# Kernel optimization log

Hardware: AMD Instinct MI355X
Metric: run time of the kernel (lower is better)

Reference implementation:

```python
import jax, jax.numpy as jnp
import numpy as np

LN_EPS = 1e-5

def _layernorm(x, g, b):
    mu = jnp.mean(x, axis=-1, keepdims=True)
    var = jnp.var(x, axis=-1, keepdims=True)
    return (x - mu) / jnp.sqrt(var + LN_EPS) * g + b

def setup_inputs() -> dict:
    key = jax.random.key(0)
    ks = jax.random.split(key, 12)
    N, D_WSI, D_OMIC, D, DH = 50000, 1024, 1577, 256, 128
    def rn(k, shape, s=0.02):
        return jax.random.normal(k, shape, jnp.float32) * s
    return {
        'wsi': jax.random.normal(ks[0], (N, D_WSI), jnp.float32),
        'x_omic': jax.random.normal(ks[1], (D_OMIC,), jnp.float32),
        # SNNOmics: Linear(1577,256)+ELU, Linear(256,256)+ELU (AlphaDropout=eval identity)
        'W1': rn(ks[2], (D_OMIC, 256)), 'b1': jnp.zeros((256,), jnp.float32),
        'W2': rn(ks[3], (256, 256)), 'b2': jnp.zeros((256,), jnp.float32),
        # wsi projection Linear(1024,256)
        'Wp': rn(ks[4], (D_WSI, D)), 'bp': jnp.zeros((D,), jnp.float32),
        # MMAttentionLayer pre-norm (dim=256)
        'ln1_g': jnp.ones((D,), jnp.float32), 'ln1_b': jnp.zeros((D,), jnp.float32),
        # to_qkv: Linear(256, 3*heads*dim_head) = Linear(256, 384), no bias (heads=1, dim_head=128)
        'Wqkv': rn(ks[5], (D, 3 * DH)),
        # FeedForward(dim=128, mult=1): LN + Linear(128,128)+GELU+Linear(128,128) (no residual)
        'ln2_g': jnp.ones((DH,), jnp.float32), 'ln2_b': jnp.zeros((DH,), jnp.float32),
        'Wf1': rn(ks[6], (DH, DH)), 'bf1': jnp.zeros((DH,), jnp.float32),
        'Wf2': rn(ks[7], (DH, DH)), 'bf2': jnp.zeros((DH,), jnp.float32),
        # final LayerNorm(128)
        'ln3_g': jnp.ones((DH,), jnp.float32), 'ln3_b': jnp.zeros((DH,), jnp.float32),
        # to_logits: Linear(256,64)+ReLU+Linear(64,4)
        'Wl1': rn(ks[8], (2 * DH, 64)), 'bl1': jnp.zeros((64,), jnp.float32),
        'Wl2': rn(ks[9], (64, 4)), 'bl2': jnp.zeros((4,), jnp.float32),
    }

def reference(wsi, x_omic, W1, b1, W2, b2, Wp, bp, ln1_g, ln1_b, Wqkv,
              ln2_g, ln2_b, Wf1, bf1, Wf2, bf2, ln3_g, ln3_b, Wl1, bl1, Wl2, bl2):
    M = 1            # num_pathways
    DH = 128         # dim_head (heads=1)
    scale = DH ** -0.5
    # SNN omics encoder -> one pathway token [1, 256]
    h = jax.nn.elu(x_omic @ W1 + b1)
    h = jax.nn.elu(h @ W2 + b2)
    h_omic = h[None, :]                              # [1, 256]
    # WSI projection -> histology tokens [N, 256]
    wsi_embed = wsi @ Wp + bp                        # [N, 256]
    tokens = jnp.concatenate([h_omic, wsi_embed], axis=0)   # [1+N, 256]
    # MMAttentionLayer: pre-norm then asymmetric pathway/histology attention
    xn = _layernorm(tokens, ln1_g, ln1_b)
    qkv = xn @ Wqkv                                  # [1+N, 384]
    q, k, v = jnp.split(qkv, 3, axis=-1)             # each [1+N, 128]
    q = q * scale
    q_p, q_h = q[:M], q[M:]                          # [1,128], [N,128]
    k_p, k_h = k[:M], k[M:]
    # cross attention: histology -> pathways (rows of length M=1)
    cross_attn_hist = q_h @ k_p.T                    # [N, 1]
    cross_attn_hist = jax.nn.softmax(cross_attn_hist, axis=-1)
    # pathway row attends to [pathways | histology]
    attn_p = q_p @ k_p.T                             # [1, 1]
    cross_attn_p = q_p @ k_h.T                       # [1, N]
    attn_ph = jax.nn.softmax(jnp.concatenate([attn_p, cross_attn_p], axis=-1), axis=-1)  # [1, 1+N]
    out_p = attn_ph @ v                              # [1, 128]
    out_h = cross_attn_hist @ v[:M]                  # [N, 128]
    out = jnp.concatenate([out_p, out_h], axis=0)    # [1+N, 128] (residual=False: no conv)
    # FeedForward (no residual add in original) + LayerNorm
    mm = _layernorm(out, ln2_g, ln2_b)
    mm = jax.nn.gelu(mm @ Wf1 + bf1, approximate=False) @ Wf2 + bf2
    mm = _layernorm(mm, ln3_g, ln3_b)                # [1+N, 128]
    paths_embed = jnp.mean(mm[:M], axis=0)           # [128]
    wsi_embed_post = jnp.mean(mm[M:], axis=0)        # [128]
    embedding = jnp.concatenate([paths_embed, wsi_embed_post])[None, :]  # [1, 256]
    logits = jax.nn.relu(embedding @ Wl1 + bl1) @ Wl2 + bl2              # [1, 4]
    prob = jax.nn.softmax(logits, axis=-1)
    return logits, prob
```

## Files before the change

kernel.cpp:

```cpp
#include <hip/hip_runtime.h>
#include <hip/hip_bf16.h>
#include <math.h>

#define LN_EPS 1e-5f

typedef unsigned short ushortT;
typedef short bf16x8 __attribute__((ext_vector_type(8)));
typedef float f32x4 __attribute__((ext_vector_type(4)));

#define WS_QP   0
#define WS_V0   128
#define WS_S0   256
#define WS_H1P  512
#define WS_PART 4608
#define PART_STRIDE 132
#define PART_M 128
#define PART_L 129
#define WS_GP   109000
#define GP_STRIDE 132
#define NCOMB   32
#define WS_WPT  131072
#define WS_WKVT 262144

__device__ __forceinline__ float elu1(float x){ return x > 0.f ? x : expm1f(x); }
__device__ __forceinline__ unsigned pk2(float lo, float hi){
  union { __hip_bfloat162 h; unsigned u; } cv;
  cv.h = __float22bfloat162_rn(make_float2(lo, hi));
  return cv.u;
}
__device__ __forceinline__ void dma16(const void* g, void* l) {
  __builtin_amdgcn_global_load_lds(
      (const __attribute__((address_space(1))) unsigned int*)g,
      (__attribute__((address_space(3))) unsigned int*)l, 16, 0, 0);
}
template<int N> __device__ __forceinline__ void vwait() {
  asm volatile("s_waitcnt vmcnt(%0)" :: "i"(N) : "memory");
}
__device__ __forceinline__ void lwait0() {
  asm volatile("s_waitcnt lgkmcnt(0)" ::: "memory");
}
__device__ __forceinline__ void sbar()   { __builtin_amdgcn_s_barrier(); }
__device__ __forceinline__ void schedb() { __builtin_amdgcn_sched_barrier(0); }

__global__ __launch_bounds__(256) void k_setup(
    const float* __restrict__ Wp, const float* __restrict__ Wqkv,
    const float* __restrict__ x, const float* __restrict__ W1, int d_omic,
    ushortT* __restrict__ wpt, ushortT* __restrict__ wkvt, float* __restrict__ ws)
{
  int bb = blockIdx.x, t = threadIdx.x;
  if (bb < 32) {
    int kc = bb, m = t, sw = (m >> 1) & 3;
    #pragma unroll
    for (int c = 0; c < 4; ++c) {
      float v[8];
      #pragma unroll
      for (int e = 0; e < 8; ++e) v[e] = Wp[(size_t)(kc * 32 + c * 8 + e) * 256 + m];
      uint4 w = make_uint4(pk2(v[0], v[1]), pk2(v[2], v[3]), pk2(v[4], v[5]), pk2(v[6], v[7]));
      *(uint4*)&wpt[kc * 8192 + m * 32 + ((c ^ sw) * 8)] = w;
    }
  } else if (bb < 40) {
    int kk = bb - 32, m = t, sw = (m >> 1) & 3;
    #pragma unroll
    for (int c = 0; c < 4; ++c) {
      float v[8];
      #pragma unroll
      for (int e = 0; e < 8; ++e) v[e] = Wqkv[(size_t)(kk * 32 + c * 8 + e) * 384 + 128 + m];
      uint4 w = make_uint4(pk2(v[0], v[1]), pk2(v[2], v[3]), pk2(v[4], v[5]), pk2(v[6], v[7]));
      *(uint4*)&wkvt[kk * 8192 + m * 32 + ((c ^ sw) * 8)] = w;
    }
  } else {
    int g = bb - 40;
    int i0 = g * 99, i1 = min(i0 + 99, d_omic);
    __shared__ float xs[112];
    for (int i = i0 + t; i < i1; i += 256) xs[i - i0] = x[i];
    __syncthreads();
    float s = 0.f;
    for (int i = i0; i < i1; i++) s = fmaf(xs[i - i0], W1[(size_t)i * 256 + t], s);
    ws[WS_H1P + g * 256 + t] = s;
  }
}

__global__ __launch_bounds__(256) void k_omic(
    const float* __restrict__ b1,
    const float* __restrict__ W2, const float* __restrict__ b2,
    const float* __restrict__ Wqkv,
    const float* __restrict__ ln1_g, const float* __restrict__ ln1_b,
    float* __restrict__ ws)
{
  __shared__ float h1[256];
  __shared__ float xn0[256];
  __shared__ float qs[128], ks[128];
  __shared__ float red[8];
  int tid = threadIdx.x, lane = tid & 63, wave = tid >> 6;

  float s = b1[tid];
  for (int g = 0; g < 16; g++) s += ws[WS_H1P + g * 256 + tid];
  h1[tid] = elu1(s);
  __syncthreads();

  s = b2[tid];
  for (int i = 0; i < 256; i++) s = fmaf(h1[i], W2[i * 256 + tid], s);
  float t0 = elu1(s);

  float ps = t0, pq = t0 * t0;
  for (int m = 1; m < 64; m <<= 1) { ps += __shfl_xor(ps, m); pq += __shfl_xor(pq, m); }
  if (lane == 0) { red[wave] = ps; red[4 + wave] = pq; }
  __syncthreads();
  float mu = (red[0] + red[1] + red[2] + red[3]) * (1.f / 256.f);
  float var = (red[4] + red[5] + red[6] + red[7]) * (1.f / 256.f) - mu * mu;
  float xn = (t0 - mu) * rsqrtf(var + LN_EPS) * ln1_g[tid] + ln1_b[tid];
  xn0[tid] = xn;
  __syncthreads();

  float a = 0.f;
  for (int j = 0; j < 256; j++) a = fmaf(xn0[j], Wqkv[j * 384 + tid], a);
  if (tid < 128) { float q = a * 0.088388347648318447f; qs[tid] = q; ws[WS_QP + tid] = q; }
  else           { ks[tid - 128] = a; }
  if (tid < 128) {
    float av = 0.f;
    for (int j = 0; j < 256; j++) av = fmaf(xn0[j], Wqkv[j * 384 + 256 + tid], av);
    ws[WS_V0 + tid] = av;
  }
  __syncthreads();
  float p = (tid < 128) ? qs[tid] * ks[tid] : 0.f;
  for (int m = 1; m < 64; m <<= 1) p += __shfl_xor(p, m);
  if (lane == 0) red[wave] = p;
  __syncthreads();
  if (tid == 0) ws[WS_S0] = red[0] + red[1] + red[2] + red[3];
}

__global__ __launch_bounds__(512, 4) void k_main(
    const float* __restrict__ wsi, int N,
    const ushortT* __restrict__ wpt, const ushortT* __restrict__ wkvt,
    const float* __restrict__ bp,
    const float* __restrict__ ln1_g, const float* __restrict__ ln1_b,
    float* __restrict__ ws)
{
  __shared__ __align__(16) char U[81920];

  const int tid = threadIdx.x;
  const int lane = tid & 63, wv = tid >> 6;
  const int l15 = lane & 15, lh = lane >> 4;
  const int cg = wv & 3, rg = wv >> 2;
  const int b = blockIdx.x, r0 = b * 128;

  int wsiSrc[2];
  #pragma unroll
  for (int i = 0; i < 2; ++i) {
    int rowL = 16 * wv + 8 * i + (lane >> 3);
    int gr = r0 + rowL; gr = (gr < N) ? gr : (N - 1);
    wsiSrc[i] = gr * 1024 + (((lane & 7) ^ (lane >> 3)) << 2);
  }
  int wptSrc[2];
  #pragma unroll
  for (int j = 0; j < 2; ++j) wptSrc[j] = (32 * wv + 16 * j) * 32 + lane * 8;

  const unsigned afslot = (unsigned)((lh ^ ((l15 >> 1) & 3)) << 4);
  const unsigned bs0 = (unsigned)(((2 * lh)     ^ (l15 & 7)) << 4);
  const unsigned bs1 = (unsigned)(((2 * lh + 1) ^ (l15 & 7)) << 4);

  const f32x4 z4 = {0.f, 0.f, 0.f, 0.f};
  f32x4 acc[4][4];
  #pragma unroll
  for (int mt = 0; mt < 4; ++mt)
    #pragma unroll
    for (int nt = 0; nt < 4; ++nt) acc[mt][nt] = z4;

  auto stageWsi = [&](int kc, int slot) {
    char* ds = U + slot * 16384 + wv * 2048;
    #pragma unroll
    for (int i = 0; i < 2; ++i) dma16(wsi + wsiSrc[i] + kc * 32, ds + i * 1024);
  };
  auto stageWpt = [&](int kc, int slot) {
    char* dw = U + 49152 + slot * 16384 + wv * 2048;
    #pragma unroll
    for (int j = 0; j < 2; ++j) dma16(wpt + wptSrc[j] + kc * 8192, dw + j * 1024);
  };

  stageWsi(0, 0); stageWpt(0, 0);
  stageWsi(1, 1); stageWpt(1, 1);
  stageWsi(2, 2);
  for (int s = 0; s < 32; ++s) {
    if (s < 30) vwait<6>(); else if (s == 30) vwait<4>(); else vwait<0>();
    sbar(); schedb();
    {
      const char* Ws = U + (s % 3) * 16384;
      const char* Wf = U + 49152 + (s & 1) * 16384;
      bf16x8 af[4], bfr[4];
      #pragma unroll
      for (int mt = 0; mt < 4; ++mt)
        af[mt] = *(const bf16x8*)(Wf + (64 * cg + 16 * mt + l15) * 64 + afslot);
      #pragma unroll
      for (int nt = 0; nt < 4; ++nt) {
        const char* p = Ws + (64 * rg + 16 * nt + l15) * 128;
        uint4 ua = *(const uint4*)(p + bs0);
        uint4 ub = *(const uint4*)(p + bs1);
        union { unsigned u[4]; bf16x8 v; } cv;
        cv.u[0] = pk2(__uint_as_float(ua.x), __uint_as_float(ua.y));
        cv.u[1] = pk2(__uint_as_float(ua.z), __uint_as_float(ua.w));
        cv.u[2] = pk2(__uint_as_float(ub.x), __uint_as_float(ub.y));
        cv.u[3] = pk2(__uint_as_float(ub.z), __uint_as_float(ub.w));
        bfr[nt] = cv.v;
      }
      #pragma unroll
      for (int mt = 0; mt < 4; ++mt)
        #pragma unroll
        for (int nt = 0; nt < 4; ++nt)
          acc[mt][nt] = __builtin_amdgcn_mfma_f32_16x16x32_bf16(af[mt], bfr[nt], acc[mt][nt], 0, 0, 0);
    }
    sbar(); schedb();
    if (s < 30) stageWpt(s + 2, s & 1);
    if (s < 29) stageWsi(s + 3, s % 3);
  }

  float* red = (float*)(U + 65536);
  float4 bp4[4], g4[4], b4[4];
  #pragma unroll
  for (int mt = 0; mt < 4; ++mt) {
    int m0 = 64 * cg + 16 * mt + 4 * lh;
    bp4[mt] = *(const float4*)&bp[m0];
    g4[mt]  = *(const float4*)&ln1_g[m0];
    b4[mt]  = *(const float4*)&ln1_b[m0];
  }
  float ps[4], pq[4];
  #pragma unroll
  for (int nt = 0; nt < 4; ++nt) { ps[nt] = 0.f; pq[nt] = 0.f; }
  #pragma unroll
  for (int mt = 0; mt < 4; ++mt) {
    const float bb4[4] = {bp4[mt].x, bp4[mt].y, bp4[mt].z, bp4[mt].w};
    #pragma unroll
    for (int nt = 0; nt < 4; ++nt)
      #pragma unroll
      for (int r = 0; r < 4; ++r) {
        float v = acc[mt][nt][r] + bb4[r];
        acc[mt][nt][r] = v;
        ps[nt] += v; pq[nt] += v * v;
      }
  }
  #pragma unroll
  for (int nt = 0; nt < 4; ++nt) {
    ps[nt] += __shfl_xor(ps[nt], 16); pq[nt] += __shfl_xor(pq[nt], 16);
    ps[nt] += __shfl_xor(ps[nt], 32); pq[nt] += __shfl_xor(pq[nt], 32);
  }
  if (lh == 0) {
    #pragma unroll
    for (int nt = 0; nt < 4; ++nt) {
      int row = 64 * rg + 16 * nt + l15;
      *(float2*)&red[row * 8 + cg * 2] = make_float2(ps[nt], pq[nt]);
    }
  }
  lwait0(); sbar(); schedb();
  float mu[4], rstd[4];
  #pragma unroll
  for (int nt = 0; nt < 4; ++nt) {
    int row = 64 * rg + 16 * nt + l15;
    float s_ = 0.f, q_ = 0.f;
    #pragma unroll
    for (int c = 0; c < 4; ++c) { s_ += red[row * 8 + c * 2]; q_ += red[row * 8 + c * 2 + 1]; }
    float m_ = s_ * (1.f / 256.f);
    float v_ = q_ * (1.f / 256.f) - m_ * m_;
    mu[nt] = m_; rstd[nt] = rsqrtf(v_ + LN_EPS);
  }
  #pragma unroll
  for (int nt = 0; nt < 4; ++nt) {
    int row = 64 * rg + 16 * nt + l15;
    unsigned rswz = (unsigned)((row & 7) << 4);
    #pragma unroll
    for (int mt = 0; mt < 4; ++mt) {
      float x0 = (acc[mt][nt][0] - mu[nt]) * rstd[nt] * g4[mt].x + b4[mt].x;
      float x1 = (acc[mt][nt][1] - mu[nt]) * rstd[nt] * g4[mt].y + b4[mt].y;
      float x2 = (acc[mt][nt][2] - mu[nt]) * rstd[nt] * g4[mt].z + b4[mt].z;
      float x3 = (acc[mt][nt][3] - mu[nt]) * rstd[nt] * g4[mt].w + b4[mt].w;
      unsigned off = (unsigned)(row * 512 + (64 * cg + 16 * mt + 4 * lh) * 2) ^ rswz;
      *(uint2*)(U + off) = make_uint2(pk2(x0, x1), pk2(x2, x3));
    }
  }
  lwait0(); sbar(); schedb();

  f32x4 acc2[4][4];
  #pragma unroll
  for (int mt = 0; mt < 4; ++mt)
    #pragma unroll
    for (int nt = 0; nt < 4; ++nt) acc2[mt][nt] = z4;
  int kvBase[4];
  #pragma unroll
  for (int mt = 0; mt < 4; ++mt) {
    int m = 64 * cg + 16 * mt + l15;
    kvBase[mt] = m * 32 + ((lh ^ ((m >> 1) & 3)) << 3);
  }
  bf16x8 gA[4], gB[4];
  #pragma unroll
  for (int mt = 0; mt < 4; ++mt) gA[mt] = *(const bf16x8*)(wkvt + kvBase[mt]);
  #pragma unroll
  for (int kp = 0; kp < 4; ++kp) {
    const int kk0 = 2 * kp, kk1 = 2 * kp + 1;
    #pragma unroll
    for (int mt = 0; mt < 4; ++mt)
      gB[mt] = *(const bf16x8*)(wkvt + kvBase[mt] + kk1 * 8192);
    {
      bf16x8 bfr[4];
      #pragma unroll
      for (int nt = 0; nt < 4; ++nt) {
        int row = 64 * rg + 16 * nt + l15;
        unsigned off = (unsigned)(row * 512 + kk0 * 64 + lh * 16) ^ (unsigned)((row & 7) << 4);
        bfr[nt] = *(const bf16x8*)(U + off);
      }
      #pragma unroll
      for (int mt = 0; mt < 4; ++mt)
        #pragma unroll
        for (int nt = 0; nt < 4; ++nt)
          acc2[mt][nt] = __builtin_amdgcn_mfma_f32_16x16x32_bf16(gA[mt], bfr[nt], acc2[mt][nt], 0, 0, 0);
    }
    if (kp < 3) {
      #pragma unroll
      for (int mt = 0; mt < 4; ++mt)
        gA[mt] = *(const bf16x8*)(wkvt + kvBase[mt] + (kk0 + 2) * 8192);
    }
    {
      bf16x8 bfr[4];
      #pragma unroll
      for (int nt = 0; nt < 4; ++nt) {
        int row = 64 * rg + 16 * nt + l15;
        unsigned off = (unsigned)(row * 512 + kk1 * 64 + lh * 16) ^ (unsigned)((row & 7) << 4);
        bfr[nt] = *(const bf16x8*)(U + off);
      }
      #pragma unroll
      for (int mt = 0; mt < 4; ++mt)
        #pragma unroll
        for (int nt = 0; nt < 4; ++nt)
          acc2[mt][nt] = __builtin_amdgcn_mfma_f32_16x16x32_bf16(gB[mt], bfr[nt], acc2[mt][nt], 0, 0, 0);
    }
  }
  sbar(); schedb();

  float* sred = (float*)U;
  float* aux  = (float*)(U + 1024);
  float* wts  = (float*)(U + 1056);
  float* vred = (float*)(U + 1600);
  float* part = ws + WS_PART + (size_t)b * PART_STRIDE;

  if (cg < 2) {
    float4 qp4[4];
    #pragma unroll
    for (int mt = 0; mt < 4; ++mt)
      qp4[mt] = *(const float4*)&ws[WS_QP + 64 * cg + 16 * mt + 4 * lh];
    float sp[4];
    #pragma unroll
    for (int nt = 0; nt < 4; ++nt) {
      float s_ = 0.f;
      #pragma unroll
      for (int mt = 0; mt < 4; ++mt) {
        s_ = fmaf(qp4[mt].x, acc2[mt][nt][0], s_);
        s_ = fmaf(qp4[mt].y, acc2[mt][nt][1], s_);
        s_ = fmaf(qp4[mt].z, acc2[mt][nt][2], s_);
        s_ = fmaf(qp4[mt].w, acc2[mt][nt][3], s_);
      }
      sp[nt] = s_;
    }
    #pragma unroll
    for (int nt = 0; nt < 4; ++nt) {
      sp[nt] += __shfl_xor(sp[nt], 16);
      sp[nt] += __shfl_xor(sp[nt], 32);
    }
    if (lh == 0) {
      #pragma unroll
      for (int nt = 0; nt < 4; ++nt) sred[cg * 128 + 64 * rg + 16 * nt + l15] = sp[nt];
    }
  }
  lwait0(); sbar(); schedb();

  float sv = -INFINITY, ev = 0.f;
  if (tid < 128) {
    sv = sred[tid] + sred[128 + tid];
    if (r0 + tid >= N) sv = -INFINITY;
  }
  float mb = sv;
  #pragma unroll
  for (int m = 1; m < 64; m <<= 1) mb = fmaxf(mb, __shfl_xor(mb, m));
  if (tid < 128 && lane == 0) aux[tid >> 6] = mb;
  lwait0(); sbar(); schedb();
  float M2 = fmaxf(aux[0], aux[1]);
  if (tid < 128) { ev = (r0 + tid < N) ? expf(sv - M2) : 0.f; wts[tid] = ev; }
  float lsum = ev;
  #pragma unroll
  for (int m = 1; m < 64; m <<= 1) lsum += __shfl_xor(lsum, m);
  if (tid < 128 && lane == 0) aux[2 + (tid >> 6)] = lsum;
  lwait0(); sbar(); schedb();
  if (tid == 0) { part[PART_M] = M2; part[PART_L] = aux[2] + aux[3]; }

  if (cg >= 2) {
    float wr[4];
    #pragma unroll
    for (int nt = 0; nt < 4; ++nt) wr[nt] = wts[64 * rg + 16 * nt + l15];
    #pragma unroll
    for (int mt = 0; mt < 4; ++mt) {
      float vs0 = 0.f, vs1 = 0.f, vs2 = 0.f, vs3 = 0.f;
      #pragma unroll
      for (int nt = 0; nt < 4; ++nt) {
        vs0 = fmaf(wr[nt], acc2[mt][nt][0], vs0);
        vs1 = fmaf(wr[nt], acc2[mt][nt][1], vs1);
        vs2 = fmaf(wr[nt], acc2[mt][nt][2], vs2);
        vs3 = fmaf(wr[nt], acc2[mt][nt][3], vs3);
      }
      #pragma unroll
      for (int m = 1; m < 16; m <<= 1) {
        vs0 += __shfl_xor(vs0, m); vs1 += __shfl_xor(vs1, m);
        vs2 += __shfl_xor(vs2, m); vs3 += __shfl_xor(vs3, m);
      }
      if (l15 == 0)
        *(float4*)&vred[128 * rg + 64 * (cg - 2) + 16 * mt + 4 * lh] =
            make_float4(vs0, vs1, vs2, vs3);
    }
  }
  lwait0(); sbar(); schedb();
  if (tid < 128) part[tid] = vred[tid] + vred[128 + tid];
}

__global__ __launch_bounds__(128) void k_fin1(float* __restrict__ ws, int NB, int chunk)
{
  int g = blockIdx.x, col = threadIdx.x;
  int c0 = g * chunk, c1 = min(c0 + chunk, NB);
  const float* part = ws + WS_PART;
  float mg = -INFINITY;
  for (int bb = c0; bb < c1; ++bb)
    mg = fmaxf(mg, part[(size_t)bb * PART_STRIDE + PART_M]);
  float a = 0.f, lg = 0.f;
  for (int bb = c0; bb < c1; ++bb) {
    float w = expf(part[(size_t)bb * PART_STRIDE + PART_M] - mg);
    a  = fmaf(part[(size_t)bb * PART_STRIDE + col], w, a);
    lg = fmaf(part[(size_t)bb * PART_STRIDE + PART_L], w, lg);
  }
  ws[WS_GP + g * GP_STRIDE + col] = a;
  if (col == 0) {
    ws[WS_GP + g * GP_STRIDE + 128] = mg;
    ws[WS_GP + g * GP_STRIDE + 129] = lg;
  }
}

__global__ __launch_bounds__(256) void k_final(
    const float* __restrict__ ws,
    const float* __restrict__ Wf1, const float* __restrict__ bf1,
    const float* __restrict__ Wf2, const float* __restrict__ bf2,
    const float* __restrict__ ln2_g, const float* __restrict__ ln2_b,
    const float* __restrict__ ln3_g, const float* __restrict__ ln3_b,
    const float* __restrict__ Wl1, const float* __restrict__ bl1,
    const float* __restrict__ Wl2, const float* __restrict__ bl2,
    float* __restrict__ out)
{
  __shared__ float rowb[2][128];
  __shared__ float mmb[2][128];
  __shared__ float red[8];
  __shared__ float emb[256];
  __shared__ float abuf[64];
  __shared__ float lbuf[4];
  __shared__ float wg[NCOMB];
  __shared__ float MLs[2];
  int tid = threadIdx.x, lane = tid & 63, wave = tid >> 6;
  float s0 = ws[WS_S0];

  if (tid == 0) {
    float M = s0;
    for (int g = 0; g < NCOMB; ++g) M = fmaxf(M, ws[WS_GP + g * GP_STRIDE + 128]);
    float L = expf(s0 - M);
    for (int g = 0; g < NCOMB; ++g)
      L = fmaf(ws[WS_GP + g * GP_STRIDE + 129], expf(ws[WS_GP + g * GP_STRIDE + 128] - M), L);
    MLs[0] = M; MLs[1] = L;
  }
  __syncthreads();
  float M = MLs[0], L = MLs[1];
  if (tid < NCOMB) wg[tid] = expf(ws[WS_GP + tid * GP_STRIDE + 128] - M);
  __syncthreads();

  if (tid < 128) {
    float v0 = ws[WS_V0 + tid];
    float a = v0 * expf(s0 - M);
    #pragma unroll
    for (int g = 0; g < NCOMB; ++g) a = fmaf(ws[WS_GP + g * GP_STRIDE + tid], wg[g], a);
    rowb[0][tid] = a / L;
    rowb[1][tid] = v0;
  }
  __syncthreads();

  int row = tid >> 7, k = tid & 127;
  float x = rowb[row][k];
  float ps = x, pq = x * x;
  for (int m = 1; m < 64; m <<= 1) { ps += __shfl_xor(ps, m); pq += __shfl_xor(pq, m); }
  __syncthreads();
  if (lane == 0) { red[wave] = ps; red[4 + wave] = pq; }
  __syncthreads();
  {
    float sum = red[row * 2] + red[row * 2 + 1];
    float sq  = red[4 + row * 2] + red[4 + row * 2 + 1];
    float mu = sum * (1.f / 128.f);
    float var = sq * (1.f / 128.f) - mu * mu;
    x = (x - mu) * rsqrtf(var + LN_EPS) * ln2_g[k] + ln2_b[k];
  }
  mmb[row][k] = x;
  __syncthreads();
  float t1 = bf1[k];
  for (int j = 0; j < 128; j++) t1 = fmaf(mmb[row][j], Wf1[j * 128 + k], t1);
  float gg = t1 * 0.5f * (1.f + erff(t1 * 0.70710678118654752f));
  __syncthreads();
  rowb[row][k] = gg;
  __syncthreads();
  float t2 = bf2[k];
  for (int j = 0; j < 128; j++) t2 = fmaf(rowb[row][j], Wf2[j * 128 + k], t2);
  ps = t2; pq = t2 * t2;
  for (int m = 1; m < 64; m <<= 1) { ps += __shfl_xor(ps, m); pq += __shfl_xor(pq, m); }
  __syncthreads();
  if (lane == 0) { red[wave] = ps; red[4 + wave] = pq; }
  __syncthreads();
  {
    float sum = red[row * 2] + red[row * 2 + 1];
    float sq  = red[4 + row * 2] + red[4 + row * 2 + 1];
    float mu = sum * (1.f / 128.f);
    float var = sq * (1.f / 128.f) - mu * mu;
    t2 = (t2 - mu) * rsqrtf(var + LN_EPS) * ln3_g[k] + ln3_b[k];
  }
  emb[row * 128 + k] = t2;
  __syncthreads();
  if (tid < 64) {
    float a = bl1[tid];
    for (int j = 0; j < 256; j++) a = fmaf(emb[j], Wl1[j * 64 + tid], a);
    abuf[tid] = fmaxf(a, 0.f);
  }
  __syncthreads();
  if (tid < 4) {
    float lg = bl2[tid];
    for (int j = 0; j < 64; j++) lg = fmaf(abuf[j], Wl2[j * 4 + tid], lg);
    lbuf[tid] = lg;
  }
  __syncthreads();
  if (tid < 4) {
    float m4 = fmaxf(fmaxf(lbuf[0], lbuf[1]), fmaxf(lbuf[2], lbuf[3]));
    float e0 = expf(lbuf[0] - m4), e1 = expf(lbuf[1] - m4);
    float e2 = expf(lbuf[2] - m4), e3 = expf(lbuf[3] - m4);
    float ssum = e0 + e1 + e2 + e3;
    out[tid] = lbuf[tid];
    out[4 + tid] = expf(lbuf[tid] - m4) / ssum;
  }
}

extern "C" void kernel_launch(void* const* d_in, const int* in_sizes, int n_in,
                              void* d_out, int out_size, void* d_ws, size_t ws_size,
                              hipStream_t stream) {
  const float* wsi    = (const float*)d_in[0];
  const float* x_omic = (const float*)d_in[1];
  const float* W1     = (const float*)d_in[2];
  const float* b1     = (const float*)d_in[3];
  const float* W2     = (const float*)d_in[4];
  const float* b2     = (const float*)d_in[5];
  const float* Wp     = (const float*)d_in[6];
  const float* bp     = (const float*)d_in[7];
  const float* ln1_g  = (const float*)d_in[8];
  const float* ln1_b  = (const float*)d_in[9];
  const float* Wqkv   = (const float*)d_in[10];
  const float* ln2_g  = (const float*)d_in[11];
  const float* ln2_b  = (const float*)d_in[12];
  const float* Wf1    = (const float*)d_in[13];
  const float* bf1    = (const float*)d_in[14];
  const float* Wf2    = (const float*)d_in[15];
  const float* bf2    = (const float*)d_in[16];
  const float* ln3_g  = (const float*)d_in[17];
  const float* ln3_b  = (const float*)d_in[18];
  const float* Wl1    = (const float*)d_in[19];
  const float* bl1    = (const float*)d_in[20];
  const float* Wl2    = (const float*)d_in[21];
  const float* bl2    = (const float*)d_in[22];
  float* ws   = (float*)d_ws;
  float* outp = (float*)d_out;
  ushortT* wpt  = (ushortT*)(ws + WS_WPT);
  ushortT* wkvt = (ushortT*)(ws + WS_WKVT);

  int N = in_sizes[0] / 1024;
  int d_omic = in_sizes[1];
  int NB = (N + 127) / 128;
  int chunk = (NB + NCOMB - 1) / NCOMB;

  k_setup<<<56, 256, 0, stream>>>(Wp, Wqkv, x_omic, W1, d_omic, wpt, wkvt, ws);
  k_omic<<<1, 256, 0, stream>>>(b1, W2, b2, Wqkv, ln1_g, ln1_b, ws);
  k_main<<<NB, 512, 0, stream>>>(wsi, N, wpt, wkvt, bp, ln1_g, ln1_b, ws);
  k_fin1<<<NCOMB, 128, 0, stream>>>(ws, NB, chunk);
  k_final<<<1, 256, 0, stream>>>(ws, Wf1, bf1, Wf2, bf2, ln2_g, ln2_b,
                                 ln3_g, ln3_b, Wl1, bl1, Wl2, bl2, outp);
}
```

Baseline: 135.9 us.

## Fold K/V projections algebraically, removing per-row second GEMM in main kernel

Computes z = Wk·q once in the omic kernel, so attention scores become dot products of the normalized 256-d rows with z. The per-block weighted sum is accumulated over the 256-d normalized rows instead of projected V, and the V projection is applied only once to the combined softmax-weighted vector in the final kernel. This removes the second per-row MFMA GEMM, the bf16 staging of normalized rows to LDS and the Wkv transpose setup. In exchange, partial buffers double in width (256 instead of 128), and scores now use fp32 normalized rows rather than bf16 products, which changes rounding slightly.

Result: slower. 141.7 us (+4.2%).

```diff
diff --git a/kernel.cpp b/kernel.cpp
--- a/kernel.cpp
+++ b/kernel.cpp
@@ -13,14 +13,14 @@
 #define WS_S0   256
 #define WS_H1P  512
 #define WS_PART 4608
-#define PART_STRIDE 132
-#define PART_M 128
-#define PART_L 129
+#define PART_STRIDE 260
+#define PART_M 256
+#define PART_L 257
+#define WS_Z    107000
 #define WS_GP   109000
-#define GP_STRIDE 132
+#define GP_STRIDE 260
 #define NCOMB   32
 #define WS_WPT  131072
-#define WS_WKVT 262144
 
 __device__ __forceinline__ float elu1(float x){ return x > 0.f ? x : expm1f(x); }
 __device__ __forceinline__ unsigned pk2(float lo, float hi){
@@ -43,9 +43,9 @@
 __device__ __forceinline__ void schedb() { __builtin_amdgcn_sched_barrier(0); }
 
 __global__ __launch_bounds__(256) void k_setup(
-    const float* __restrict__ Wp, const float* __restrict__ Wqkv,
+    const float* __restrict__ Wp,
     const float* __restrict__ x, const float* __restrict__ W1, int d_omic,
-    ushortT* __restrict__ wpt, ushortT* __restrict__ wkvt, float* __restrict__ ws)
+    ushortT* __restrict__ wpt, float* __restrict__ ws)
 {
   int bb = blockIdx.x, t = threadIdx.x;
   if (bb < 32) {
@@ -58,18 +58,8 @@
       uint4 w = make_uint4(pk2(v[0], v[1]), pk2(v[2], v[3]), pk2(v[4], v[5]), pk2(v[6], v[7]));
       *(uint4*)&wpt[kc * 8192 + m * 32 + ((c ^ sw) * 8)] = w;
     }
-  } else if (bb < 40) {
-    int kk = bb - 32, m = t, sw = (m >> 1) & 3;
-    #pragma unroll
-    for (int c = 0; c < 4; ++c) {
-      float v[8];
-      #pragma unroll
-      for (int e = 0; e < 8; ++e) v[e] = Wqkv[(size_t)(kk * 32 + c * 8 + e) * 384 + 128 + m];
-      uint4 w = make_uint4(pk2(v[0], v[1]), pk2(v[2], v[3]), pk2(v[4], v[5]), pk2(v[6], v[7]));
-      *(uint4*)&wkvt[kk * 8192 + m * 32 + ((c ^ sw) * 8)] = w;
-    }
   } else {
-    int g = bb - 40;
+    int g = bb - 32;
     int i0 = g * 99, i1 = min(i0 + 99, d_omic);
     __shared__ float xs[112];
     for (int i = i0 + t; i < i1; i += 256) xs[i - i0] = x[i];
@@ -127,11 +117,23 @@
   if (lane == 0) red[wave] = p;
   __syncthreads();
   if (tid == 0) ws[WS_S0] = red[0] + red[1] + red[2] + red[3];
+
+  float zv = 0.f;
+  #pragma unroll 4
+  for (int d = 0; d < 128; d += 4) {
+    float4 q4 = *(const float4*)&qs[d];
+    const float* wr_ = &Wqkv[tid * 384 + 128 + d];
+    zv = fmaf(q4.x, wr_[0], zv);
+    zv = fmaf(q4.y, wr_[1], zv);
+    zv = fmaf(q4.z, wr_[2], zv);
+    zv = fmaf(q4.w, wr_[3], zv);
+  }
+  ws[WS_Z + tid] = zv;
 }
 
 __global__ __launch_bounds__(512, 4) void k_main(
     const float* __restrict__ wsi, int N,
-    const ushortT* __restrict__ wpt, const ushortT* __restrict__ wkvt,
+    const ushortT* __restrict__ wpt,
     const float* __restrict__ bp,
     const float* __restrict__ ln1_g, const float* __restrict__ ln1_b,
     float* __restrict__ ws)
@@ -159,12 +161,12 @@
   const unsigned bs0 = (unsigned)(((2 * lh)     ^ (l15 & 7)) << 4);
   const unsigned bs1 = (unsigned)(((2 * lh + 1) ^ (l15 & 7)) << 4);
 
-  const f32x4 z4 = {0.f, 0.f, 0.f, 0.f};
+  const f32x4 z4i = {0.f, 0.f, 0.f, 0.f};
   f32x4 acc[4][4];
   #pragma unroll
   for (int mt = 0; mt < 4; ++mt)
     #pragma unroll
-    for (int nt = 0; nt < 4; ++nt) acc[mt][nt] = z4;
+    for (int nt = 0; nt < 4; ++nt) acc[mt][nt] = z4i;
 
   auto stageWsi = [&](int kc, int slot) {
     char* ds = U + slot * 16384 + wv * 2048;
@@ -261,99 +263,38 @@
     float v_ = q_ * (1.f / 256.f) - m_ * m_;
     mu[nt] = m_; rstd[nt] = rsqrtf(v_ + LN_EPS);
   }
-  #pragma unroll
-  for (int nt = 0; nt < 4; ++nt) {
-    int row = 64 * rg + 16 * nt + l15;
-    unsigned rswz = (unsigned)((row & 7) << 4);
-    #pragma unroll
-    for (int mt = 0; mt < 4; ++mt) {
-      float x0 = (acc[mt][nt][0] - mu[nt]) * rstd[nt] * g4[mt].x + b4[mt].x;
-      float x1 = (acc[mt][nt][1] - mu[nt]) * rstd[nt] * g4[mt].y + b4[mt].y;
-      float x2 = (acc[mt][nt][2] - mu[nt]) * rstd[nt] * g4[mt].z + b4[mt].z;
-      float x3 = (acc[mt][nt][3] - mu[nt]) * rstd[nt] * g4[mt].w + b4[mt].w;
-      unsigned off = (unsigned)(row * 512 + (64 * cg + 16 * mt + 4 * lh) * 2) ^ rswz;
-      *(uint2*)(U + off) = make_uint2(pk2(x0, x1), pk2(x2, x3));
-    }
-  }
-  lwait0(); sbar(); schedb();
-
-  f32x4 acc2[4][4];
+
   #pragma unroll
   for (int mt = 0; mt < 4; ++mt)
     #pragma unroll
-    for (int nt = 0; nt < 4; ++nt) acc2[mt][nt] = z4;
-  int kvBase[4];
-  #pragma unroll
-  for (int mt = 0; mt < 4; ++mt) {
-    int m = 64 * cg + 16 * mt + l15;
-    kvBase[mt] = m * 32 + ((lh ^ ((m >> 1) & 3)) << 3);
-  }
-  bf16x8 gA[4], gB[4];
-  #pragma unroll
-  for (int mt = 0; mt < 4; ++mt) gA[mt] = *(const bf16x8*)(wkvt + kvBase[mt]);
-  #pragma unroll
-  for (int kp = 0; kp < 4; ++kp) {
-    const int kk0 = 2 * kp, kk1 = 2 * kp + 1;
+    for (int nt = 0; nt < 4; ++nt) {
+      acc[mt][nt][0] = (acc[mt][nt][0] - mu[nt]) * rstd[nt] * g4[mt].x + b4[mt].x;
+      acc[mt][nt][1] = (acc[mt][nt][1] - mu[nt]) * rstd[nt] * g4[mt].y + b4[mt].y;
+      acc[mt][nt][2] = (acc[mt][nt][2] - mu[nt]) * rstd[nt] * g4[mt].z + b4[mt].z;
+      acc[mt][nt][3] = (acc[mt][nt][3] - mu[nt]) * rstd[nt] * g4[mt].w + b4[mt].w;
+    }
+
+  float* sred = (float*)U;
+  float* aux  = (float*)(U + 2048);
+  float* wts  = (float*)(U + 2112);
+  float* vred = (float*)(U + 3072);
+  float* part = ws + WS_PART + (size_t)b * PART_STRIDE;
+
+  {
+    float4 zf[4];
     #pragma unroll
     for (int mt = 0; mt < 4; ++mt)
-      gB[mt] = *(const bf16x8*)(wkvt + kvBase[mt] + kk1 * 8192);
-    {
-      bf16x8 bfr[4];
-      #pragma unroll
-      for (int nt = 0; nt < 4; ++nt) {
-        int row = 64 * rg + 16 * nt + l15;
-        unsigned off = (unsigned)(row * 512 + kk0 * 64 + lh * 16) ^ (unsigned)((row & 7) << 4);
-        bfr[nt] = *(const bf16x8*)(U + off);
-      }
-      #pragma unroll
-      for (int mt = 0; mt < 4; ++mt)
-        #pragma unroll
-        for (int nt = 0; nt < 4; ++nt)
-          acc2[mt][nt] = __builtin_amdgcn_mfma_f32_16x16x32_bf16(gA[mt], bfr[nt], acc2[mt][nt], 0, 0, 0);
-    }
-    if (kp < 3) {
-      #pragma unroll
-      for (int mt = 0; mt < 4; ++mt)
-        gA[mt] = *(const bf16x8*)(wkvt + kvBase[mt] + (kk0 + 2) * 8192);
-    }
-    {
-      bf16x8 bfr[4];
-      #pragma unroll
-      for (int nt = 0; nt < 4; ++nt) {
-        int row = 64 * rg + 16 * nt + l15;
-        unsigned off = (unsigned)(row * 512 + kk1 * 64 + lh * 16) ^ (unsigned)((row & 7) << 4);
-        bfr[nt] = *(const bf16x8*)(U + off);
-      }
-      #pragma unroll
-      for (int mt = 0; mt < 4; ++mt)
-        #pragma unroll
-        for (int nt = 0; nt < 4; ++nt)
-          acc2[mt][nt] = __builtin_amdgcn_mfma_f32_16x16x32_bf16(gB[mt], bfr[nt], acc2[mt][nt], 0, 0, 0);
-    }
-  }
-  sbar(); schedb();
-
-  float* sred = (float*)U;
-  float* aux  = (float*)(U + 1024);
-  float* wts  = (float*)(U + 1056);
-  float* vred = (float*)(U + 1600);
-  float* part = ws + WS_PART + (size_t)b * PART_STRIDE;
-
-  if (cg < 2) {
-    float4 qp4[4];
-    #pragma unroll
-    for (int mt = 0; mt < 4; ++mt)
-      qp4[mt] = *(const float4*)&ws[WS_QP + 64 * cg + 16 * mt + 4 * lh];
+      zf[mt] = *(const float4*)&ws[WS_Z + 64 * cg + 16 * mt + 4 * lh];
     float sp[4];
     #pragma unroll
     for (int nt = 0; nt < 4; ++nt) {
       float s_ = 0.f;
       #pragma unroll
       for (int mt = 0; mt < 4; ++mt) {
-        s_ = fmaf(qp4[mt].x, acc2[mt][nt][0], s_);
-        s_ = fmaf(qp4[mt].y, acc2[mt][nt][1], s_);
-        s_ = fmaf(qp4[mt].z, acc2[mt][nt][2], s_);
-        s_ = fmaf(qp4[mt].w, acc2[mt][nt][3], s_);
+        s_ = fmaf(zf[mt].x, acc[mt][nt][0], s_);
+        s_ = fmaf(zf[mt].y, acc[mt][nt][1], s_);
+        s_ = fmaf(zf[mt].z, acc[mt][nt][2], s_);
+        s_ = fmaf(zf[mt].w, acc[mt][nt][3], s_);
       }
       sp[nt] = s_;
     }
@@ -371,7 +312,7 @@
 
   float sv = -INFINITY, ev = 0.f;
   if (tid < 128) {
-    sv = sred[tid] + sred[128 + tid];
+    sv = sred[tid] + sred[128 + tid] + sred[256 + tid] + sred[384 + tid];
     if (r0 + tid >= N) sv = -INFINITY;
   }
   float mb = sv;
@@ -388,7 +329,7 @@
   lwait0(); sbar(); schedb();
   if (tid == 0) { part[PART_M] = M2; part[PART_L] = aux[2] + aux[3]; }
 
-  if (cg >= 2) {
+  {
     float wr[4];
     #pragma unroll
     for (int nt = 0; nt < 4; ++nt) wr[nt] = wts[64 * rg + 16 * nt + l15];
@@ -397,10 +338,10 @@
       float vs0 = 0.f, vs1 = 0.f, vs2 = 0.f, vs3 = 0.f;
       #pragma unroll
       for (int nt = 0; nt < 4; ++nt) {
-        vs0 = fmaf(wr[nt], acc2[mt][nt][0], vs0);
-        vs1 = fmaf(wr[nt], acc2[mt][nt][1], vs1);
-        vs2 = fmaf(wr[nt], acc2[mt][nt][2], vs2);
-        vs3 = fmaf(wr[nt], acc2[mt][nt][3], vs3);
+        vs0 = fmaf(wr[nt], acc[mt][nt][0], vs0);
+        vs1 = fmaf(wr[nt], acc[mt][nt][1], vs1);
+        vs2 = fmaf(wr[nt], acc[mt][nt][2], vs2);
+        vs3 = fmaf(wr[nt], acc[mt][nt][3], vs3);
       }
       #pragma unroll
       for (int m = 1; m < 16; m <<= 1) {
@@ -408,15 +349,15 @@
         vs2 += __shfl_xor(vs2, m); vs3 += __shfl_xor(vs3, m);
       }
       if (l15 == 0)
-        *(float4*)&vred[128 * rg + 64 * (cg - 2) + 16 * mt + 4 * lh] =
+        *(float4*)&vred[256 * rg + 64 * cg + 16 * mt + 4 * lh] =
             make_float4(vs0, vs1, vs2, vs3);
     }
   }
   lwait0(); sbar(); schedb();
-  if (tid < 128) part[tid] = vred[tid] + vred[128 + tid];
-}
-
-__global__ __launch_bounds__(128) void k_fin1(float* __restrict__ ws, int NB, int chunk)
+  if (tid < 256) part[tid] = vred[tid] + vred[256 + tid];
+}
+
+__global__ __launch_bounds__(256) void k_fin1(float* __restrict__ ws, int NB, int chunk)
 {
   int g = blockIdx.x, col = threadIdx.x;
   int c0 = g * chunk, c1 = min(c0 + chunk, NB);
@@ -432,13 +373,13 @@
   }
   ws[WS_GP + g * GP_STRIDE + col] = a;
   if (col == 0) {
-    ws[WS_GP + g * GP_STRIDE + 128] = mg;
-    ws[WS_GP + g * GP_STRIDE + 129] = lg;
+    ws[WS_GP + g * GP_STRIDE + PART_M] = mg;
+    ws[WS_GP + g * GP_STRIDE + PART_L] = lg;
   }
 }
 
 __global__ __launch_bounds__(256) void k_final(
-    const float* __restrict__ ws,
+    const float* __restrict__ ws, const float* __restrict__ Wqkv,
     const float* __restrict__ Wf1, const float* __restrict__ bf1,
     const float* __restrict__ Wf2, const float* __restrict__ bf2,
     const float* __restrict__ ln2_g, const float* __restrict__ ln2_b,
@@ -455,27 +396,36 @@
   __shared__ float lbuf[4];
   __shared__ float wg[NCOMB];
   __shared__ float MLs[2];
+  __shared__ float Ybuf[256];
   int tid = threadIdx.x, lane = tid & 63, wave = tid >> 6;
   float s0 = ws[WS_S0];
 
   if (tid == 0) {
     float M = s0;
-    for (int g = 0; g < NCOMB; ++g) M = fmaxf(M, ws[WS_GP + g * GP_STRIDE + 128]);
+    for (int g = 0; g < NCOMB; ++g) M = fmaxf(M, ws[WS_GP + g * GP_STRIDE + PART_M]);
     float L = expf(s0 - M);
     for (int g = 0; g < NCOMB; ++g)
-      L = fmaf(ws[WS_GP + g * GP_STRIDE + 129], expf(ws[WS_GP + g * GP_STRIDE + 128] - M), L);
+      L = fmaf(ws[WS_GP + g * GP_STRIDE + PART_L], expf(ws[WS_GP + g * GP_STRIDE + PART_M] - M), L);
     MLs[0] = M; MLs[1] = L;
   }
   __syncthreads();
   float M = MLs[0], L = MLs[1];
-  if (tid < NCOMB) wg[tid] = expf(ws[WS_GP + tid * GP_STRIDE + 128] - M);
+  if (tid < NCOMB) wg[tid] = expf(ws[WS_GP + tid * GP_STRIDE + PART_M] - M);
+  __syncthreads();
+
+  {
+    float y = 0.f;
+    #pragma unroll
+    for (int g = 0; g < NCOMB; ++g) y = fmaf(ws[WS_GP + g * GP_STRIDE + tid], wg[g], y);
+    Ybuf[tid] = y;
+  }
   __syncthreads();
 
   if (tid < 128) {
     float v0 = ws[WS_V0 + tid];
     float a = v0 * expf(s0 - M);
-    #pragma unroll
-    for (int g = 0; g < NCOMB; ++g) a = fmaf(ws[WS_GP + g * GP_STRIDE + tid], wg[g], a);
+    for (int c = 0; c < 256; ++c)
+      a = fmaf(Ybuf[c], Wqkv[c * 384 + 256 + tid], a);
     rowb[0][tid] = a / L;
     rowb[1][tid] = v0;
   }
@@ -569,18 +519,17 @@
   const float* bl2    = (const float*)d_in[22];
   float* ws   = (float*)d_ws;
   float* outp = (float*)d_out;
-  ushortT* wpt  = (ushortT*)(ws + WS_WPT);
-  ushortT* wkvt = (ushortT*)(ws + WS_WKVT);
+  ushortT* wpt = (ushortT*)(ws + WS_WPT);
 
   int N = in_sizes[0] / 1024;
   int d_omic = in_sizes[1];
   int NB = (N + 127) / 128;
   int chunk = (NB + NCOMB - 1) / NCOMB;
 
-  k_setup<<<56, 256, 0, stream>>>(Wp, Wqkv, x_omic, W1, d_omic, wpt, wkvt, ws);
+  k_setup<<<48, 256, 0, stream>>>(Wp, x_omic, W1, d_omic, wpt, ws);
   k_omic<<<1, 256, 0, stream>>>(b1, W2, b2, Wqkv, ln1_g, ln1_b, ws);
-  k_main<<<NB, 512, 0, stream>>>(wsi, N, wpt, wkvt, bp, ln1_g, ln1_b, ws);
-  k_fin1<<<NCOMB, 128, 0, stream>>>(ws, NB, chunk);
-  k_final<<<1, 256, 0, stream>>>(ws, Wf1, bf1, Wf2, bf2, ln2_g, ln2_b,
+  k_main<<<NB, 512, 0, stream>>>(wsi, N, wpt, bp, ln1_g, ln1_b, ws);
+  k_fin1<<<NCOMB, 256, 0, stream>>>(ws, NB, chunk);
+  k_final<<<1, 256, 0, stream>>>(ws, Wqkv, Wf1, bf1, Wf2, bf2, ln2_g, ln2_b,
                                  ln3_g, ln3_b, Wl1, bl1, Wl2, bl2, outp);
 }
```
